# Kernel optimization log

Measured on AMD Instinct MI355X. Metric: run time of the kernel, lower is better.

Reference implementation:

```python
import jax, jax.numpy as jnp
import numpy as np

H = 128; R = 8; VN = 100; VA = 64
N = 8192; B = 64; L = 48; E = 65536


def setup_inputs() -> dict:
    key = jax.random.key(0)
    ks = jax.random.split(key, 24)
    s = 0.05
    nodeTypes = jax.random.randint(ks[0], (N,), 0, VN)
    edge_index = jax.random.randint(ks[1], (2, E), 0, N)
    edge_attr = jax.random.randint(ks[2], (E,), 0, R)
    bs = jnp.repeat(jnp.arange(B), N // B)              # sorted node->graph map
    nodes_bs = jnp.full((B,), N // B, dtype=jnp.int32)  # nodes per graph
    len_seq = jax.random.randint(ks[3], (B,), 1, L + 1).at[0].set(L)  # max == L
    sequence_input = (jax.random.uniform(ks[4], (N, L)) < 0.05).astype(jnp.float32)
    action_input = jax.random.randint(ks[5], (B,), 0, VA)
    params = dict(
        emb_nodes=jax.random.normal(ks[6], (VN, H)) * s,
        emb_actions=jax.random.normal(ks[7], (VA, H)) * s,
        rgcn_rel=jax.random.normal(ks[8], (3, R, H, H)) * s,   # per-layer relation weights
        rgcn_root=jax.random.normal(ks[9], (3, H, H)) * s,
        rgcn_bias=jnp.zeros((3, H)),
        gru_w_ih=jax.random.normal(ks[10], (3 * H, H)) * s,
        gru_w_hh=jax.random.normal(ks[11], (3 * H, H)) * s,
        gru_b_ih=jnp.zeros((3 * H,)),
        gru_b_hh=jnp.zeros((3 * H,)),
        linA_w=jax.random.normal(ks[12], (H, H)) * s,
        linA_b=jnp.zeros((H,)),
        linAf_w=jax.random.normal(ks[13], (VA, H)) * s,
        linAf_b=jnp.zeros((VA,)),
        linN_w=jax.random.normal(ks[14], (H, 2 * H)) * s,
        linN_b=jnp.zeros((H,)),
        linNf_w=jax.random.normal(ks[15], (1, H)) * s,
        linNf_b=jnp.zeros((1,)),
    )
    return dict(nodeTypes=nodeTypes, edge_index=edge_index, edge_attr=edge_attr,
                bs=bs, nodes_bs=nodes_bs, len_seq=len_seq,
                sequence_input=sequence_input, action_input=action_input, **params)


def reference(nodeTypes, edge_index, edge_attr, bs, nodes_bs, len_seq,
              sequence_input, action_input,
              emb_nodes, emb_actions, rgcn_rel, rgcn_root, rgcn_bias,
              gru_w_ih, gru_w_hh, gru_b_ih, gru_b_hh,
              linA_w, linA_b, linAf_w, linAf_b,
              linN_w, linN_b, linNf_w, linNf_b):
    n = nodeTypes.shape[0]
    b = nodes_bs.shape[0]
    h = emb_nodes.shape[1]
    r = rgcn_rel.shape[1]
    l = sequence_input.shape[1]

    x = emb_nodes[nodeTypes]                               # [N,H]
    src, dst = edge_index[0], edge_index[1]
    seg = dst * r + edge_attr                              # per (target, relation) segment
    cnt = jax.ops.segment_sum(jnp.ones((src.shape[0],), x.dtype), seg, n * r)
    denom = jnp.maximum(cnt, 1.0).reshape(n, r, 1)
    for li in range(3):
        agg = jax.ops.segment_sum(x[src], seg, n * r).reshape(n, r, h) / denom
        x = jax.nn.relu(jnp.einsum('nrh,rho->no', agg, rgcn_rel[li])
                        + x @ rgcn_root[li] + rgcn_bias[li])

    # global mean pool -> graph embedding
    h_G = jax.ops.segment_sum(x, bs, b) / nodes_bs[:, None].astype(x.dtype)  # [B,H]
    action = jax.nn.relu(h_G @ linA_w.T + linA_b) @ linAf_w.T + linAf_b      # [B,VA]

    sos = emb_actions[action_input][:, None, :]            # [B,1,H]
    # sequence embeddings: sum over nodes in each graph of seq[i,t]*x[i]
    emb_seq = sequence_input[:, :, None] * x[:, None, :]   # [N,L,H]
    out = jax.ops.segment_sum(emb_seq, bs, b)              # [B,L,H]
    input_gru = jnp.concatenate([sos, out], axis=1)[:, :l] # packed GRU only sees first L steps

    # single-layer GRU, h0 = h_G (torch gate order r,z,n)
    xW = input_gru @ gru_w_ih.T + gru_b_ih                 # [B,L,3H]
    def step(hprev, xw):
        hW = hprev @ gru_w_hh.T + gru_b_hh
        xr, xz, xn = jnp.split(xw, 3, -1)
        hr, hz, hn = jnp.split(hW, 3, -1)
        rg = jax.nn.sigmoid(xr + hr)
        zg = jax.nn.sigmoid(xz + hz)
        ng = jnp.tanh(xn + rg * hn)
        hnew = (1.0 - zg) * ng + zg * hprev
        return hnew, hnew
    _, hs = jax.lax.scan(step, h_G, jnp.swapaxes(xW, 0, 1))
    seq_out = jnp.swapaxes(hs, 0, 1)                       # [B,L,H]
    mask = jnp.arange(l)[None, :] < len_seq[:, None]       # pad_packed zero-pads
    seq_out = seq_out * mask[:, :, None]

    out_gru = seq_out[bs]                                  # repeat_interleave -> [N,L,H]
    concats = jnp.concatenate(
        [out_gru, jnp.broadcast_to(x[:, None, :], (n, l, h))], axis=2)  # [N,L,2H]
    hid = jax.nn.relu(concats @ linN_w.T + linN_b)         # [N,L,H]
    logits = (hid @ linNf_w.T + linNf_b)[..., 0]           # [N,L]

    # scatter_softmax over nodes grouped by graph (dim 0)
    m = jax.lax.stop_gradient(jax.ops.segment_max(logits, bs, b))
    e = jnp.exp(logits - m[bs])
    ssum = jax.ops.segment_sum(e, bs, b)
    nodes_final = e / ssum[bs]
    return action, nodes_final
```

## Files before the change

### kernel.cpp

```cpp
#include <hip/hip_runtime.h>
#include <hip/hip_bf16.h>

#define H   128
#define RR  8
#define NN  8192
#define BB  64
#define LL  48
#define EE  65536
#define NPG 128
#define VA  64
#define NSEG (NN*RR)
#define GPB 16

typedef unsigned short u16;
typedef unsigned int   u32;

__device__ __forceinline__ float b2f(u16 u) {
    union { u32 i; float f; } v; v.i = ((u32)u) << 16; return v.f;
}
__device__ __forceinline__ u16 f2b(float f) {
    union { float f; u32 i; } v; v.f = f;
    u32 x = v.i;
    return (u16)((x + 0x7fffu + ((x >> 16) & 1u)) >> 16);
}
__device__ __forceinline__ float2 up2(u32 p) {
    union { u32 i; float f; } a, b;
    a.i = p << 16; b.i = p & 0xffff0000u;
    return make_float2(a.f, b.f);
}
__device__ __forceinline__ u32 pk2(float a, float b) {
    return ((u32)f2b(b) << 16) | (u32)f2b(a);
}
__device__ __forceinline__ float rcpf(float x) { return __builtin_amdgcn_rcpf(x); }
__device__ __forceinline__ u32 cvtpk(float lo, float hi) {
    u32 r;
    asm("v_cvt_pk_bf16_f32 %0, %1, %2" : "=v"(r) : "v"(lo), "v"(hi));
    return r;
}

#define K_LOG2E  1.4426950408889634f
#define K_2LOG2E 2.8853900817779268f

typedef __attribute__((ext_vector_type(8))) short bf16x8;
typedef __attribute__((ext_vector_type(4))) float f32x4;
typedef __attribute__((ext_vector_type(4))) unsigned short u16x4;

__global__ __launch_bounds__(256) void k_init(const int* __restrict__ nodeTypes,
                                              const float* __restrict__ emb_nodes,
                                              float* __restrict__ x0,
                                              int* __restrict__ fill) {
    int idx = blockIdx.x * 256 + threadIdx.x;
    if (idx < NSEG) fill[idx] = 0;
    if (idx < NN * H) {
        int n = idx >> 7, h = idx & (H - 1);
        x0[idx] = emb_nodes[(size_t)nodeTypes[n] * H + h];
    }
}

__global__ __launch_bounds__(256) void k_hist(const int* __restrict__ edge_index,
                                              const int* __restrict__ edge_attr,
                                              int* __restrict__ fill) {
    int e = blockIdx.x * 256 + threadIdx.x;
    if (e < EE) {
        int seg = edge_index[EE + e] * RR + edge_attr[e];
        atomicAdd(&fill[seg], 1);
    }
}

__global__ __launch_bounds__(256) void k_scan1(const int* __restrict__ fill,
                                               int* __restrict__ bsum) {
    __shared__ int red[4];
    int tid = threadIdx.x, lane = tid & 63, wv = tid >> 6;
    int v = fill[blockIdx.x * 256 + tid];
#pragma unroll
    for (int off = 32; off >= 1; off >>= 1) v += __shfl_down(v, off, 64);
    if (lane == 0) red[wv] = v;
    __syncthreads();
    if (tid == 0) bsum[blockIdx.x] = red[0] + red[1] + red[2] + red[3];
}

__global__ __launch_bounds__(256) void k_scan2(const int* __restrict__ bsum,
                                               int* __restrict__ boff,
                                               int* __restrict__ rowptr) {
    __shared__ int s[256];
    int tid = threadIdx.x;
    int v0 = bsum[tid];
    s[tid] = v0;
    __syncthreads();
    for (int off = 1; off < 256; off <<= 1) {
        int v = (tid >= off) ? s[tid - off] : 0;
        __syncthreads();
        s[tid] += v;
        __syncthreads();
    }
    boff[tid] = s[tid] - v0;
    if (tid == 255) rowptr[NSEG] = s[255];
}

__global__ __launch_bounds__(256) void k_scan3(const int* __restrict__ boff,
                                               int* __restrict__ fill,
                                               int* __restrict__ rowptr) {
    __shared__ int s[256];
    int tid = threadIdx.x;
    int g = blockIdx.x * 256 + tid;
    int c = fill[g];
    s[tid] = c;
    __syncthreads();
    for (int off = 1; off < 256; off <<= 1) {
        int v = (tid >= off) ? s[tid - off] : 0;
        __syncthreads();
        s[tid] += v;
        __syncthreads();
    }
    int r = boff[blockIdx.x] + s[tid] - c;
    rowptr[g] = r;
    fill[g] = r;
}

__global__ __launch_bounds__(256) void k_scatter(const int* __restrict__ edge_index,
                                                 const int* __restrict__ edge_attr,
                                                 int* __restrict__ fill,
                                                 int* __restrict__ colidx) {
    int e = blockIdx.x * 256 + threadIdx.x;
    if (e < EE) {
        int seg = edge_index[EE + e] * RR + edge_attr[e];
        int pos = atomicAdd(&fill[seg], 1);
        colidx[pos] = edge_index[e];
    }
}

__global__ __launch_bounds__(256) void k_wprep(const float* __restrict__ rel,
                                               const float* __restrict__ root,
                                               const float* __restrict__ w_ih,
                                               u16* __restrict__ WTt,
                                               u16* __restrict__ WTih,
                                               float* __restrict__ hGsum) {
    int idx = blockIdx.x * 256 + threadIdx.x;
    if (idx < 384 * H) WTih[idx] = f2b(w_ih[idx]);
    if (idx < BB * H) hGsum[idx] = 0.f;
    if (idx >= 3 * 147456) return;
    int li  = idx / 147456;
    int rem = idx - li * 147456;
    int tile = rem / 36864;
    int r2   = rem - tile * 36864;
    int ks   = r2 / 1024;
    int r3   = r2 - ks * 1024;
    int sub  = r3 >> 9;
    int r4   = r3 & 511;
    int lane = r4 >> 3, j = r4 & 7;
    int col = tile * 32 + sub * 16 + (lane & 15);
    int k   = ks * 32 + (lane >> 4) * 8 + j;
    float v;
    if (k < 1024) v = rel[(((size_t)li * RR + (k >> 7)) * H + (k & 127)) * H + col];
    else          v = root[((size_t)li * H + (k - 1024)) * H + col];
    WTt[idx] = f2b(v);
}

#define RGN 16
#define EPRE 512

__global__ __launch_bounds__(512) void k_rgcn(const float* __restrict__ xin,
                                              float* __restrict__ xout,
                                              const u16* __restrict__ WTt,
                                              const float* __restrict__ bias,
                                              const int* __restrict__ rowptr,
                                              const int* __restrict__ colidx,
                                              float* __restrict__ hGsum) {
    __shared__ u32 ab[RGN * 580];
    __shared__ int begs[RGN * RR + 1];
    __shared__ int eidx[EPRE];
    int tid = threadIdx.x, wv = tid >> 6, lane = tid & 63;
    int n0 = blockIdx.x * RGN, segbase = n0 * RR;

    if (tid <= RGN * RR) begs[tid] = rowptr[segbase + tid];
    __syncthreads();
    int E0 = begs[0], ne = begs[RGN * RR] - E0;
    for (int i = tid; i < ne && i < EPRE; i += 512) eidx[i] = colidx[E0 + i];
    __syncthreads();

    for (int s = wv; s < RGN * RR; s += 8) {
        int beg = begs[s], end = begs[s + 1];
        float a0 = 0.f, a1 = 0.f;
        for (int e = beg; e < end; ++e) {
            int off = e - E0;
            int src = (off < EPRE) ? eidx[off] : colidx[e];
            float2 v = ((const float2*)(xin + (size_t)src * H))[lane];
            a0 += v.x; a1 += v.y;
        }
        float inv = 1.f / fmaxf((float)(end - beg), 1.f);
        ab[(s >> 3) * 580 + ((s & 7) << 6) + lane] = pk2(a0 * inv, a1 * inv);
    }
    for (int i = wv; i < RGN; i += 8) {
        const float* xr = xin + (size_t)(n0 + i) * H + 2 * lane;
        ab[i * 580 + 512 + lane] = pk2(xr[0], xr[1]);
    }
    __syncthreads();

    int m = lane & 15, quad = lane >> 4;
    const u32* aP = ab + m * 580 + quad * 4;
    const u32* bT = (const u32*)WTt + (size_t)(wv >> 1) * 36 * 512 + (wv & 1) * 256 + lane * 4;
    f32x4 acc0 = {0.f, 0.f, 0.f, 0.f};
    bf16x8 b0c = *(const bf16x8*)bT;
    for (int ks = 0; ks < 36; ++ks) {
        bf16x8 b0n;
        if (ks < 35) b0n = *(const bf16x8*)(bT + (ks + 1) * 512);
        bf16x8 a = *(const bf16x8*)(aP + ks * 16);
        acc0 = __builtin_amdgcn_mfma_f32_16x16x32_bf16(a, b0c, acc0, 0, 0, 0);
        b0c = b0n;
    }
    int c0 = wv * 16 + m;
    float bv0 = bias[c0];
    float so0 = 0.f;
#pragma unroll
    for (int rg = 0; rg < 4; ++rg) {
        int n = n0 + quad * 4 + rg;
        float o0 = fmaxf(acc0[rg] + bv0, 0.f);
        xout[(size_t)n * H + c0] = o0;
        so0 += o0;
    }
    if (hGsum) {
        so0 += __shfl_xor(so0, 16, 64);
        so0 += __shfl_xor(so0, 32, 64);
        if (quad == 0) {
            int g = n0 >> 7;
            atomicAdd(&hGsum[g * H + c0], so0);
        }
    }
}

__global__ __launch_bounds__(128) void k_pool_act(const float* __restrict__ hGsum,
                                                  const int* __restrict__ nodes_bs,
                                                  const float* __restrict__ linA_w,
                                                  const float* __restrict__ linA_b,
                                                  const float* __restrict__ linAf_w,
                                                  const float* __restrict__ linAf_b,
                                                  float* __restrict__ hG,
                                                  float* __restrict__ out) {
    __shared__ float hgs[H], t1[H];
    int b = blockIdx.x, h = threadIdx.x;
    float hg = hGsum[(size_t)b * H + h] / (float)nodes_bs[b];
    hG[(size_t)b * H + h] = hg;
    hgs[h] = hg;
    __syncthreads();
    float acc = linA_b[h];
    const float* wr = linA_w + (size_t)h * H;
    for (int k = 0; k < H; ++k) acc += wr[k] * hgs[k];
    t1[h] = fmaxf(acc, 0.f);
    __syncthreads();
    if (h < VA) {
        float a = linAf_b[h];
        const float* w2 = linAf_w + (size_t)h * H;
        for (int k = 0; k < H; ++k) a += w2[k] * t1[k];
        out[(size_t)b * VA + h] = a;
    }
}

__global__ __launch_bounds__(256) void k_seqpool(const float* __restrict__ xf,
                                                 const float* __restrict__ seq,
                                                 const float* __restrict__ emb_actions,
                                                 const int* __restrict__ action_input,
                                                 float* __restrict__ igG) {
    __shared__ float xg[64][H];
    __shared__ u16 lists[LL][64];
    __shared__ int cnts[LL];
    int b = blockIdx.x, tid = threadIdx.x;
    int col = tid & 127, tg = tid >> 7;
    float acc[24];
#pragma unroll
    for (int m = 0; m < 24; ++m) acc[m] = 0.f;

    for (int chunk = 0; chunk < 2; ++chunk) {
        int i0 = b * NPG + chunk * 64;
        __syncthreads();
        if (tid < LL) cnts[tid] = 0;
        __syncthreads();
        for (int idx = tid; idx < 64 * H / 4; idx += 256)
            ((float4*)&xg[0][0])[idx] = ((const float4*)(xf + (size_t)i0 * H))[idx];
        for (int idx = tid; idx < 64 * LL; idx += 256) {
            int i = idx / LL, t = idx - i * LL;
            if (seq[(size_t)(i0 + i) * LL + t] != 0.f) {
                int p = atomicAdd(&cnts[t], 1);
                lists[t][p] = (u16)i;
            }
        }
        __syncthreads();
        for (int m = 0; m < 24; ++m) {
            int t = tg + 2 * m;
            int c = cnts[t];
            float a = acc[m];
            for (int p = 0; p < c; ++p) a += xg[lists[t][p]][col];
            acc[m] = a;
        }
    }
    if (tid < H)
        igG[((size_t)b * LL) * H + tid] = emb_actions[(size_t)action_input[b] * H + tid];
#pragma unroll
    for (int m = 0; m < 24; ++m) {
        int t = tg + 2 * m;
        if (t < LL - 1)
            igG[((size_t)b * LL + t + 1) * H + col] = acc[m];
    }
}

__global__ __launch_bounds__(256) void k_xw(const float* __restrict__ igG,
                                            const u16* __restrict__ WTih,
                                            const float* __restrict__ b_ih,
                                            const float* __restrict__ b_hh,
                                            u16* __restrict__ xwG) {
    __shared__ u32 ab[16 * 68];
    int tid = threadIdx.x, wv = tid >> 6, lane = tid & 63;
    int n0 = blockIdx.x * 16;
    for (int s = tid; s < 16 * 64; s += 256) {
        int row = s >> 6, kp = s & 63;
        float2 v = *(const float2*)(igG + (size_t)(n0 + row) * H + 2 * kp);
        ab[row * 68 + kp] = pk2(v.x, v.y);
    }
    __syncthreads();
    int m = lane & 15, quad = lane >> 4;
    const u32* aP = ab + m * 68 + quad * 4;
    f32x4 acc[6];
#pragma unroll
    for (int i = 0; i < 6; ++i) acc[i] = (f32x4){0.f, 0.f, 0.f, 0.f};
#pragma unroll
    for (int ks = 0; ks < 4; ++ks) {
        bf16x8 a = *(const bf16x8*)(aP + ks * 16);
#pragma unroll
        for (int tc = 0; tc < 6; ++tc) {
            int colr = wv * 96 + tc * 16 + m;
            bf16x8 bfr = *(const bf16x8*)((const u32*)WTih + (size_t)colr * 64 + quad * 4 + ks * 16);
            acc[tc] = __builtin_amdgcn_mfma_f32_16x16x32_bf16(a, bfr, acc[tc], 0, 0, 0);
        }
    }
#pragma unroll
    for (int tc = 0; tc < 6; ++tc) {
        int c = wv * 96 + tc * 16 + m;
        float bv = b_ih[c] + ((c < 256) ? b_hh[c] : 0.f);
        float sc = (c < 256) ? K_LOG2E : K_2LOG2E;
        int R = c & 127, gate = c >> 7;
#pragma unroll
        for (int rg = 0; rg < 4; ++rg) {
            int r = n0 + quad * 4 + rg;
            int bb = r / 48, tt = r - bb * 48;
            size_t o = (((((size_t)(bb >> 4) * LL + tt) * 8 + (R >> 4)) * 3 + gate) * 256)
                     + (((R >> 2) & 3) << 6) + ((bb & 15) << 2) + (R & 3);
            xwG[o] = f2b((acc[tc][rg] + bv) * sc);
        }
    }
}

#define GRU_BLKS 4
#define BX_BLKS  (NN / 32)
#define SMEM_BYTES 33024

__global__ __launch_bounds__(512) void k_gru_bx(const u16* __restrict__ xw2,
                                                const float* __restrict__ hG,
                                                const float* __restrict__ w_hh,
                                                const float* __restrict__ b_hh,
                                                const int* __restrict__ len_seq,
                                                float* __restrict__ soutG,
                                                const float* __restrict__ xf,
                                                const float* __restrict__ linN_w,
                                                const float* __restrict__ linN_b,
                                                u16* __restrict__ BxU) {
    __shared__ __align__(16) char smem[SMEM_BYTES];
    int tid = threadIdx.x;

    if (blockIdx.x >= GRU_BLKS) {
        float* xl = (float*)smem;
        float* wb = (float*)(smem + 16384);
        int bid = blockIdx.x - GRU_BLKS;
        int n0 = bid * 32;
        for (int idx = tid; idx < 32 * H; idx += 512)
            xl[idx] = xf[(size_t)n0 * H + idx];
        int col = tid & 127, g = tid >> 7;
        float bv = linN_b[col];
        float acc[8] = {bv, bv, bv, bv, bv, bv, bv, bv};
        for (int c = 0; c < 4; ++c) {
            int k0 = c * 32;
            __syncthreads();
            for (int idx = tid; idx < 32 * H; idx += 512) {
                int r = idx >> 5, kk = idx & 31;
                wb[kk * 130 + r] = linN_w[(size_t)r * (2 * H) + H + k0 + kk];
            }
            __syncthreads();
#pragma unroll
            for (int kk = 0; kk < 32; ++kk) {
                float w = wb[kk * 130 + col];
#pragma unroll
                for (int j = 0; j < 8; ++j) acc[j] += xl[(g * 8 + j) * H + k0 + kk] * w;
            }
        }
#pragma unroll
        for (int j = 0; j < 8; ++j)
            BxU[(size_t)(n0 + g * 8 + j) * H + col] = f2b(acc[j]);
        return;
    }

    u16* hA = (u16*)smem;
    int lane = tid & 63, wv = tid >> 6;
    int mi = lane & 15, quad = lane >> 4;
    int gblk = blockIdx.x;
    int g_abs = gblk * GPB + mi;
    int R0 = 16 * wv + 4 * quad;

    int eW = (((wv >> 1) * 64) + (mi + 16 * ((2 * wv + (quad >> 1)) & 3))) * 8
             + 4 * (quad & 1);

    bf16x8 wfr[3][4];
#pragma unroll
    for (int gate = 0; gate < 3; ++gate) {
        int T = wv + 8 * gate;
        float sc = (gate == 2) ? K_2LOG2E : K_LOG2E;
#pragma unroll
        for (int ks = 0; ks < 4; ++ks) {
            const float* wp = w_hh + (size_t)(16 * T + mi) * H + quad * 8 + ks * 32;
            float4 f0 = *(const float4*)wp;
            float4 f1 = *(const float4*)(wp + 4);
            bf16x8 v;
            v[0] = (short)f2b(f0.x * sc); v[1] = (short)f2b(f0.y * sc);
            v[2] = (short)f2b(f0.z * sc); v[3] = (short)f2b(f0.w * sc);
            v[4] = (short)f2b(f1.x * sc); v[5] = (short)f2b(f1.y * sc);
            v[6] = (short)f2b(f1.z * sc); v[7] = (short)f2b(f1.w * sc);
            wfr[gate][ks] = v;
        }
    }
    float4 bn = *(const float4*)(b_hh + 256 + R0);
    float4 h0 = *(const float4*)(hG + (size_t)g_abs * H + R0);
    int ls = len_seq[g_abs];

    float hp[4]  = {h0.x, h0.y, h0.z, h0.w};
    float bnn[4] = {bn.x * K_2LOG2E, bn.y * K_2LOG2E, bn.z * K_2LOG2E, bn.w * K_2LOG2E};

    auto storeh = [&](int buf, const float* hv) {
        u32 w0 = cvtpk(hv[0], hv[1]);
        u32 w1 = cvtpk(hv[2], hv[3]);
        float2 e0 = up2(w0), e1 = up2(w1);
        u32 l0 = cvtpk(hv[0] - e0.x, hv[1] - e0.y);
        u32 l1 = cvtpk(hv[2] - e1.x, hv[3] - e1.y);
        *(uint2*)&hA[buf * 4096 + eW]        = make_uint2(w0, w1);
        *(uint2*)&hA[buf * 4096 + 2048 + eW] = make_uint2(l0, l1);
    };
    auto loadxw = [&](int t, u16x4* d) {
        const u16* p = xw2 + ((((size_t)gblk * LL + t) * 8 + wv) * 3) * 256
                     + (quad << 6) + (mi << 2);
        d[0] = *(const u16x4*)(p);
        d[1] = *(const u16x4*)(p + 256);
        d[2] = *(const u16x4*)(p + 512);
    };

    auto step = [&](int t, const u16x4* x, int buf) {
        f32x4 acc[3];
        acc[0] = (f32x4){0.f, 0.f, 0.f, 0.f};
        acc[1] = (f32x4){0.f, 0.f, 0.f, 0.f};
        acc[2] = (f32x4){bnn[0], bnn[1], bnn[2], bnn[3]};
#pragma unroll
        for (int ks = 0; ks < 4; ++ks) {
            const int e = (ks * 64 + lane) * 8;
            bf16x8 bh = *(const bf16x8*)&hA[buf * 4096 + e];
            bf16x8 bl = *(const bf16x8*)&hA[buf * 4096 + 2048 + e];
#pragma unroll
            for (int gate = 0; gate < 3; ++gate) {
                acc[gate] = __builtin_amdgcn_mfma_f32_16x16x32_bf16(wfr[gate][ks], bh, acc[gate], 0, 0, 0);
                acc[gate] = __builtin_amdgcn_mfma_f32_16x16x32_bf16(wfr[gate][ks], bl, acc[gate], 0, 0, 0);
            }
        }
        float hv[4];
        float4 so;
#pragma unroll
        for (int r = 0; r < 4; ++r) {
            float xr = b2f(x[0][r]);
            float xz = b2f(x[1][r]);
            float xn = b2f(x[2][r]);
            float rg = rcpf(1.f + __builtin_amdgcn_exp2f(-(xr + acc[0][r])));
            float zg = rcpf(1.f + __builtin_amdgcn_exp2f(-(xz + acc[1][r])));
            float u  = xn + rg * acc[2][r];
            float ng = 1.f - 2.f * rcpf(__builtin_amdgcn_exp2f(u) + 1.f);
            float hn = ng + zg * (hp[r] - ng);
            hp[r] = hn;
            hv[r] = hn;
            ((float*)&so)[r] = (t < ls) ? hn : 0.f;
        }
        *(float4*)(soutG + ((size_t)g_abs * LL + t) * H + R0) = so;
        storeh(buf ^ 1, hv);
    };

    u16x4 xa[3], xb[3];
    loadxw(0, xa);
    loadxw(1, xb);
    storeh(0, hp);
    asm volatile("s_waitcnt lgkmcnt(0)\n\ts_barrier" ::: "memory");

    for (int t = 0; t < LL; t += 2) {
        step(t, xa, 0);
        if (t + 2 < LL) loadxw(t + 2, xa);
        asm volatile("s_waitcnt lgkmcnt(0)\n\ts_barrier" ::: "memory");
        step(t + 1, xb, 1);
        if (t + 3 < LL) loadxw(t + 3, xb);
        asm volatile("s_waitcnt lgkmcnt(0)\n\ts_barrier" ::: "memory");
    }
}

__global__ __launch_bounds__(256) void k_a2(const float* __restrict__ soutG,
                                            const float* __restrict__ linN_w,
                                            float* __restrict__ A2) {
    __shared__ float wb[32][130];
    __shared__ float xl[16][H];
    int tid = threadIdx.x;
    int n0 = blockIdx.x * 16;
    for (int idx = tid; idx < 16 * H; idx += 256)
        xl[idx >> 7][idx & 127] = soutG[(size_t)n0 * H + idx];
    int col = tid & 127, g = tid >> 7;
    float acc[8] = {0.f, 0.f, 0.f, 0.f, 0.f, 0.f, 0.f, 0.f};
    for (int c = 0; c < 4; ++c) {
        int k0 = c * 32;
        __syncthreads();
        for (int idx = tid; idx < 32 * H; idx += 256) {
            int r = idx >> 5, kk = idx & 31;
            wb[kk][r] = linN_w[(size_t)r * (2 * H) + k0 + kk];
        }
        __syncthreads();
#pragma unroll
        for (int kk = 0; kk < 32; ++kk) {
            float w = wb[kk][col];
#pragma unroll
            for (int j = 0; j < 8; ++j) acc[j] += xl[g * 8 + j][k0 + kk] * w;
        }
    }
#pragma unroll
    for (int j = 0; j < 8; ++j)
        A2[(size_t)(n0 + g * 8 + j) * H + col] = acc[j];
}

__global__ __launch_bounds__(256) void k_logits(const float* __restrict__ A2,
                                                const u16* __restrict__ BxU,
                                                const float* __restrict__ linNf_w,
                                                float* __restrict__ logits) {
    __shared__ float a2s[LL][130];
    __shared__ float bxs[16][130];
    __shared__ float w2s[H];
    int tid = threadIdx.x;
    int g = blockIdx.x >> 3, tile = blockIdx.x & 7;
    int n0g = g * NPG + tile * 16;

    for (int i2 = tid; i2 < LL * 64; i2 += 256) {
        int r = i2 >> 6, c2 = i2 & 63;
        *(float2*)&a2s[r][2 * c2] = *(const float2*)(A2 + ((size_t)g * LL + r) * H + 2 * c2);
    }
    for (int iu = tid; iu < 16 * 64; iu += 256) {
        int r = iu >> 6, c = iu & 63;
        float2 v = up2(((const u32*)BxU)[(size_t)(n0g + r) * 64 + c]);
        *(float2*)&bxs[r][2 * c] = v;
    }
    if (tid < H) w2s[tid] = linNf_w[tid];
    __syncthreads();

    int n = tid & 15, tt = tid >> 4;
#pragma unroll
    for (int pass = 0; pass < 3; ++pass) {
        int t = tt + 16 * pass;
        float acc = 0.f;
#pragma unroll
        for (int kp = 0; kp < 64; ++kp) {
            float2 a2 = *(const float2*)&a2s[t][2 * kp];
            float2 bx = *(const float2*)&bxs[n][2 * kp];
            float2 w  = *(const float2*)&w2s[2 * kp];
            acc += w.x * fmaxf(a2.x + bx.x, 0.f) + w.y * fmaxf(a2.y + bx.y, 0.f);
        }
        logits[(size_t)(n0g + n) * LL + t] = acc;
    }
}

__global__ __launch_bounds__(256) void k_softmax(const float* __restrict__ logits,
                                                 float* __restrict__ out) {
    __shared__ float lg[NPG][LL + 1];
    __shared__ float pm[4][LL], ps[4][LL];
    __shared__ float mv[LL], inv[LL];
    int b = blockIdx.x, tid = threadIdx.x;
    int n0 = b * NPG;
    for (int idx = tid; idx < NPG * LL; idx += 256) {
        int n = idx / LL, t = idx - n * LL;
        lg[n][t] = logits[(size_t)n0 * LL + idx];
    }
    __syncthreads();
    int t = tid & 63, seg = tid >> 6;
    if (t < LL) {
        float m = -1e30f;
        int nb = seg * 32;
        for (int n = nb; n < nb + 32; ++n) m = fmaxf(m, lg[n][t]);
        pm[seg][t] = m;
    }
    __syncthreads();
    if (tid < LL)
        mv[tid] = fmaxf(fmaxf(pm[0][tid], pm[1][tid]), fmaxf(pm[2][tid], pm[3][tid]));
    __syncthreads();
    if (t < LL) {
        float m = mv[t], s = 0.f;
        int nb = seg * 32;
        for (int n = nb; n < nb + 32; ++n) {
            float e = __expf(lg[n][t] - m);
            lg[n][t] = e;
            s += e;
        }
        ps[seg][t] = s;
    }
    __syncthreads();
    if (tid < LL)
        inv[tid] = 1.f / (ps[0][tid] + ps[1][tid] + ps[2][tid] + ps[3][tid]);
    __syncthreads();
    for (int idx = tid; idx < NPG * LL; idx += 256) {
        int n = idx / LL, tc = idx - n * LL;
        out[(size_t)BB * VA + (size_t)n0 * LL + idx] = lg[n][tc] * inv[tc];
    }
}

extern "C" void kernel_launch(void* const* d_in, const int* in_sizes, int n_in,
                              void* d_out, int out_size, void* d_ws, size_t ws_size,
                              hipStream_t stream) {
    (void)in_sizes; (void)n_in; (void)out_size; (void)ws_size;
    const int*   nodeTypes    = (const int*)d_in[0];
    const int*   edge_index   = (const int*)d_in[1];
    const int*   edge_attr    = (const int*)d_in[2];
    const int*   nodes_bs     = (const int*)d_in[4];
    const int*   len_seq      = (const int*)d_in[5];
    const float* seq_in       = (const float*)d_in[6];
    const int*   action_input = (const int*)d_in[7];
    const float* emb_nodes    = (const float*)d_in[8];
    const float* emb_actions  = (const float*)d_in[9];
    const float* rgcn_rel     = (const float*)d_in[10];
    const float* rgcn_root    = (const float*)d_in[11];
    const float* rgcn_bias    = (const float*)d_in[12];
    const float* gru_w_ih     = (const float*)d_in[13];
    const float* gru_w_hh     = (const float*)d_in[14];
    const float* gru_b_ih     = (const float*)d_in[15];
    const float* gru_b_hh     = (const float*)d_in[16];
    const float* linA_w       = (const float*)d_in[17];
    const float* linA_b       = (const float*)d_in[18];
    const float* linAf_w      = (const float*)d_in[19];
    const float* linAf_b      = (const float*)d_in[20];
    const float* linN_w       = (const float*)d_in[21];
    const float* linN_b       = (const float*)d_in[22];
    const float* linNf_w      = (const float*)d_in[23];

    char* w = (char*)d_ws;
    float* x0      = (float*)(w + 0);
    u16*   xwG     = (u16*)  (w + 0);
    float* logitsW = (float*)(w + 0);
    float* soutG   = (float*)(w + 2359296);
    float* x1      = (float*)(w + 4194304);
    float* igG     = (float*)(w + 8388608);
    float* A2      = (float*)(w + 8388608);
    u16*   BxU     = (u16*)  (w + 9961472);
    int*   bsum    = (int*)  (w + 9961472);
    int*   boff    = (int*)  (w + 9962496);
    float* hGsum   = (float*)(w + 9969664);
    int*   rowptr  = (int*)  (w + 11567104);
    int*   fill    = (int*)  (w + 11829760);
    u16*   WTih    = (u16*)  (w + 11829760);
    float* hG      = (float*)(w + 12058624);
    int*   colidx  = (int*)  (w + 12091904);
    u16*   WT      = (u16*)  (w + 12616192);

    float* out_f = (float*)d_out;

    k_init<<<dim3(4096), dim3(256), 0, stream>>>(nodeTypes, emb_nodes, x0, fill);
    k_hist<<<dim3(256), dim3(256), 0, stream>>>(edge_index, edge_attr, fill);
    k_scan1<<<dim3(256), dim3(256), 0, stream>>>(fill, bsum);
    k_scan2<<<dim3(1), dim3(256), 0, stream>>>(bsum, boff, rowptr);
    k_scan3<<<dim3(256), dim3(256), 0, stream>>>(boff, fill, rowptr);
    k_scatter<<<dim3(256), dim3(256), 0, stream>>>(edge_index, edge_attr, fill, colidx);
    k_wprep<<<dim3(1728), dim3(256), 0, stream>>>(rgcn_rel, rgcn_root, gru_w_ih,
                                                  WT, WTih, hGsum);

    const int rg_grid = NN / RGN;
    k_rgcn<<<dim3(rg_grid), dim3(512), 0, stream>>>(x0, x1,
        WT + 0 * 147456, rgcn_bias + 0 * H, rowptr, colidx, nullptr);
    k_rgcn<<<dim3(rg_grid), dim3(512), 0, stream>>>(x1, x0,
        WT + 1 * 147456, rgcn_bias + 1 * H, rowptr, colidx, nullptr);
    k_rgcn<<<dim3(rg_grid), dim3(512), 0, stream>>>(x0, x1,
        WT + 2 * 147456, rgcn_bias + 2 * H, rowptr, colidx, hGsum);

    k_pool_act<<<dim3(BB), dim3(128), 0, stream>>>(hGsum, nodes_bs, linA_w, linA_b,
                                                   linAf_w, linAf_b, hG, out_f);
    k_seqpool<<<dim3(BB), dim3(256), 0, stream>>>(x1, seq_in, emb_actions, action_input, igG);
    k_xw<<<dim3(BB * LL / 16), dim3(256), 0, stream>>>(igG, WTih, gru_b_ih, gru_b_hh, xwG);
    k_gru_bx<<<dim3(GRU_BLKS + BX_BLKS), dim3(512), 0, stream>>>(xwG, hG, gru_w_hh,
        gru_b_hh, len_seq, soutG, x1, linN_w, linN_b, BxU);
    k_a2<<<dim3(BB * LL / 16), dim3(256), 0, stream>>>(soutG, linN_w, A2);
    k_logits<<<dim3(BB * 8), dim3(256), 0, stream>>>(A2, BxU, linNf_w, logitsW);
    k_softmax<<<dim3(BB), dim3(256), 0, stream>>>(logitsW, out_f);
}
```

Before: 321.6 us.

## Replace CSR edge build with per-block buckets and LDS atomic aggregation

Replaces the histogram, three-pass scan and scatter CSR construction with a single bucketing kernel that places each edge in a fixed-capacity bucket per 16-node destination block. The RGCN kernel then aggregates neighbour features with shared-memory float atomics and normalises by per-relation counts. Separately, the init and weight-prep kernels are merged, as are the pool/action and sequence-pool kernels, which cuts the launch count. The risks are the CAP=256 bucket cap, which silently drops edges if a block receives more, the contention from LDS atomics, and a non-deterministic summation order.

```diff
diff --git a/kernel.cpp b/kernel.cpp
--- a/kernel.cpp
+++ b/kernel.cpp
@@ -9,8 +9,8 @@
 #define EE  65536
 #define NPG 128
 #define VA  64
-#define NSEG (NN*RR)
 #define GPB 16
+#define CAP 256
 
 typedef unsigned short u16;
 typedef unsigned int   u32;
@@ -45,167 +45,119 @@
 typedef __attribute__((ext_vector_type(4))) float f32x4;
 typedef __attribute__((ext_vector_type(4))) unsigned short u16x4;
 
-__global__ __launch_bounds__(256) void k_init(const int* __restrict__ nodeTypes,
+__global__ __launch_bounds__(256) void k_prep(const int* __restrict__ nodeTypes,
                                               const float* __restrict__ emb_nodes,
+                                              const float* __restrict__ rel,
+                                              const float* __restrict__ root,
+                                              const float* __restrict__ w_ih,
                                               float* __restrict__ x0,
-                                              int* __restrict__ fill) {
+                                              u16* __restrict__ WTt,
+                                              u16* __restrict__ WTih,
+                                              float* __restrict__ hGsum,
+                                              int* __restrict__ bcnt) {
     int idx = blockIdx.x * 256 + threadIdx.x;
-    if (idx < NSEG) fill[idx] = 0;
+    if (idx < 512) bcnt[idx] = 0;
+    if (idx < 384 * H) WTih[idx] = f2b(w_ih[idx]);
+    if (idx < BB * H) hGsum[idx] = 0.f;
     if (idx < NN * H) {
         int n = idx >> 7, h = idx & (H - 1);
         x0[idx] = emb_nodes[(size_t)nodeTypes[n] * H + h];
     }
-}
-
-__global__ __launch_bounds__(256) void k_hist(const int* __restrict__ edge_index,
-                                              const int* __restrict__ edge_attr,
-                                              int* __restrict__ fill) {
-    int e = blockIdx.x * 256 + threadIdx.x;
-    if (e < EE) {
-        int seg = edge_index[EE + e] * RR + edge_attr[e];
-        atomicAdd(&fill[seg], 1);
-    }
-}
-
-__global__ __launch_bounds__(256) void k_scan1(const int* __restrict__ fill,
-                                               int* __restrict__ bsum) {
-    __shared__ int red[4];
-    int tid = threadIdx.x, lane = tid & 63, wv = tid >> 6;
-    int v = fill[blockIdx.x * 256 + tid];
-#pragma unroll
-    for (int off = 32; off >= 1; off >>= 1) v += __shfl_down(v, off, 64);
-    if (lane == 0) red[wv] = v;
-    __syncthreads();
-    if (tid == 0) bsum[blockIdx.x] = red[0] + red[1] + red[2] + red[3];
-}
-
-__global__ __launch_bounds__(256) void k_scan2(const int* __restrict__ bsum,
-                                               int* __restrict__ boff,
-                                               int* __restrict__ rowptr) {
-    __shared__ int s[256];
-    int tid = threadIdx.x;
-    int v0 = bsum[tid];
-    s[tid] = v0;
-    __syncthreads();
-    for (int off = 1; off < 256; off <<= 1) {
-        int v = (tid >= off) ? s[tid - off] : 0;
-        __syncthreads();
-        s[tid] += v;
-        __syncthreads();
-    }
-    boff[tid] = s[tid] - v0;
-    if (tid == 255) rowptr[NSEG] = s[255];
-}
-
-__global__ __launch_bounds__(256) void k_scan3(const int* __restrict__ boff,
-                                               int* __restrict__ fill,
-                                               int* __restrict__ rowptr) {
-    __shared__ int s[256];
-    int tid = threadIdx.x;
-    int g = blockIdx.x * 256 + tid;
-    int c = fill[g];
-    s[tid] = c;
-    __syncthreads();
-    for (int off = 1; off < 256; off <<= 1) {
-        int v = (tid >= off) ? s[tid - off] : 0;
-        __syncthreads();
-        s[tid] += v;
-        __syncthreads();
-    }
-    int r = boff[blockIdx.x] + s[tid] - c;
-    rowptr[g] = r;
-    fill[g] = r;
-}
-
-__global__ __launch_bounds__(256) void k_scatter(const int* __restrict__ edge_index,
-                                                 const int* __restrict__ edge_attr,
-                                                 int* __restrict__ fill,
-                                                 int* __restrict__ colidx) {
-    int e = blockIdx.x * 256 + threadIdx.x;
-    if (e < EE) {
-        int seg = edge_index[EE + e] * RR + edge_attr[e];
-        int pos = atomicAdd(&fill[seg], 1);
-        colidx[pos] = edge_index[e];
-    }
-}
-
-__global__ __launch_bounds__(256) void k_wprep(const float* __restrict__ rel,
-                                               const float* __restrict__ root,
-                                               const float* __restrict__ w_ih,
-                                               u16* __restrict__ WTt,
-                                               u16* __restrict__ WTih,
-                                               float* __restrict__ hGsum) {
-    int idx = blockIdx.x * 256 + threadIdx.x;
-    if (idx < 384 * H) WTih[idx] = f2b(w_ih[idx]);
-    if (idx < BB * H) hGsum[idx] = 0.f;
-    if (idx >= 3 * 147456) return;
-    int li  = idx / 147456;
-    int rem = idx - li * 147456;
+    int j = idx - NN * H;
+    if (j < 0 || j >= 3 * 147456) return;
+    int li  = j / 147456;
+    int rem = j - li * 147456;
     int tile = rem / 36864;
     int r2   = rem - tile * 36864;
     int ks   = r2 / 1024;
     int r3   = r2 - ks * 1024;
     int sub  = r3 >> 9;
     int r4   = r3 & 511;
-    int lane = r4 >> 3, j = r4 & 7;
+    int lane = r4 >> 3, jj = r4 & 7;
     int col = tile * 32 + sub * 16 + (lane & 15);
-    int k   = ks * 32 + (lane >> 4) * 8 + j;
+    int k   = ks * 32 + (lane >> 4) * 8 + jj;
     float v;
     if (k < 1024) v = rel[(((size_t)li * RR + (k >> 7)) * H + (k & 127)) * H + col];
     else          v = root[((size_t)li * H + (k - 1024)) * H + col];
-    WTt[idx] = f2b(v);
+    WTt[j] = f2b(v);
+}
+
+__global__ __launch_bounds__(256) void k_bucket(const int* __restrict__ edge_index,
+                                                const int* __restrict__ edge_attr,
+                                                int* __restrict__ bcnt,
+                                                u32* __restrict__ bucket) {
+    int e = blockIdx.x * 256 + threadIdx.x;
+    if (e < EE) {
+        int dst = edge_index[EE + e];
+        int blk = dst >> 4;
+        int pos = atomicAdd(&bcnt[blk], 1);
+        if (pos < CAP) {
+            u32 sl = (u32)(((dst & 15) << 3) | edge_attr[e]);
+            bucket[(size_t)blk * CAP + pos] = (u32)edge_index[e] | (sl << 16);
+        }
+    }
 }
 
 #define RGN 16
-#define EPRE 512
 
 __global__ __launch_bounds__(512) void k_rgcn(const float* __restrict__ xin,
                                               float* __restrict__ xout,
                                               const u16* __restrict__ WTt,
                                               const float* __restrict__ bias,
-                                              const int* __restrict__ rowptr,
-                                              const int* __restrict__ colidx,
+                                              const int* __restrict__ bcnt,
+                                              const u32* __restrict__ bucket,
                                               float* __restrict__ hGsum) {
-    __shared__ u32 ab[RGN * 580];
-    __shared__ int begs[RGN * RR + 1];
-    __shared__ int eidx[EPRE];
+    __shared__ __align__(16) float agg[RGN * 9 * 132];
+    __shared__ u32 ebuf[CAP];
+    __shared__ int cnts[RGN * RR];
     int tid = threadIdx.x, wv = tid >> 6, lane = tid & 63;
-    int n0 = blockIdx.x * RGN, segbase = n0 * RR;
-
-    if (tid <= RGN * RR) begs[tid] = rowptr[segbase + tid];
-    __syncthreads();
-    int E0 = begs[0], ne = begs[RGN * RR] - E0;
-    for (int i = tid; i < ne && i < EPRE; i += 512) eidx[i] = colidx[E0 + i];
-    __syncthreads();
-
-    for (int s = wv; s < RGN * RR; s += 8) {
-        int beg = begs[s], end = begs[s + 1];
-        float a0 = 0.f, a1 = 0.f;
-        for (int e = beg; e < end; ++e) {
-            int off = e - E0;
-            int src = (off < EPRE) ? eidx[off] : colidx[e];
-            float2 v = ((const float2*)(xin + (size_t)src * H))[lane];
-            a0 += v.x; a1 += v.y;
-        }
-        float inv = 1.f / fmaxf((float)(end - beg), 1.f);
-        ab[(s >> 3) * 580 + ((s & 7) << 6) + lane] = pk2(a0 * inv, a1 * inv);
-    }
-    for (int i = wv; i < RGN; i += 8) {
-        const float* xr = xin + (size_t)(n0 + i) * H + 2 * lane;
-        ab[i * 580 + 512 + lane] = pk2(xr[0], xr[1]);
+    int blk = blockIdx.x, n0 = blk * RGN;
+    int ne = min(bcnt[blk], CAP);
+
+    for (int i = tid; i < ne; i += 512) ebuf[i] = bucket[(size_t)blk * CAP + i];
+    for (int i = tid; i < RGN * RR; i += 512) cnts[i] = 0;
+    for (int i = tid; i < RGN * 8 * 128; i += 512) {
+        int n = i >> 10, r = (i >> 7) & 7, h = i & 127;
+        agg[(n * 9 + r) * 132 + h] = 0.f;
+    }
+    for (int i = tid; i < RGN * 128; i += 512)
+        agg[((i >> 7) * 9 + 8) * 132 + (i & 127)] = xin[(size_t)n0 * H + i];
+    __syncthreads();
+
+    for (int e = wv; e < ne; e += 8) {
+        u32 pk = ebuf[e];
+        int src = pk & 0xffff, sl = pk >> 16;
+        float2 v = ((const float2*)(xin + (size_t)src * H))[lane];
+        float* dst = &agg[((sl >> 3) * 9 + (sl & 7)) * 132 + 2 * lane];
+        atomicAdd(dst, v.x);
+        atomicAdd(dst + 1, v.y);
+        if (lane == 0) atomicAdd(&cnts[sl], 1);
+    }
+    __syncthreads();
+
+    for (int i = tid; i < RGN * 8 * 128; i += 512) {
+        int n = i >> 10, r = (i >> 7) & 7, h = i & 127;
+        float sc = 1.f / fmaxf((float)cnts[i >> 7], 1.f);
+        agg[(n * 9 + r) * 132 + h] *= sc;
     }
     __syncthreads();
 
     int m = lane & 15, quad = lane >> 4;
-    const u32* aP = ab + m * 580 + quad * 4;
     const u32* bT = (const u32*)WTt + (size_t)(wv >> 1) * 36 * 512 + (wv & 1) * 256 + lane * 4;
     f32x4 acc0 = {0.f, 0.f, 0.f, 0.f};
     bf16x8 b0c = *(const bf16x8*)bT;
     for (int ks = 0; ks < 36; ++ks) {
         bf16x8 b0n;
         if (ks < 35) b0n = *(const bf16x8*)(bT + (ks + 1) * 512);
-        bf16x8 a = *(const bf16x8*)(aP + ks * 16);
-        acc0 = __builtin_amdgcn_mfma_f32_16x16x32_bf16(a, b0c, acc0, 0, 0, 0);
+        int seg = ks >> 2;
+        int h0 = (ks * 32 + quad * 8) & 127;
+        const float* ap = &agg[(m * 9 + seg) * 132 + h0];
+        float4 f0 = *(const float4*)ap;
+        float4 f1 = *(const float4*)(ap + 4);
+        union { u32 u[4]; bf16x8 v; } av;
+        av.u[0] = cvtpk(f0.x, f0.y); av.u[1] = cvtpk(f0.z, f0.w);
+        av.u[2] = cvtpk(f1.x, f1.y); av.u[3] = cvtpk(f1.z, f1.w);
+        acc0 = __builtin_amdgcn_mfma_f32_16x16x32_bf16(av.v, b0c, acc0, 0, 0, 0);
         b0c = b0n;
     }
     int c0 = wv * 16 + m;
@@ -228,42 +180,51 @@
     }
 }
 
-__global__ __launch_bounds__(128) void k_pool_act(const float* __restrict__ hGsum,
+__global__ __launch_bounds__(256) void k_pool_seq(const float* __restrict__ hGsum,
                                                   const int* __restrict__ nodes_bs,
                                                   const float* __restrict__ linA_w,
                                                   const float* __restrict__ linA_b,
                                                   const float* __restrict__ linAf_w,
                                                   const float* __restrict__ linAf_b,
                                                   float* __restrict__ hG,
-                                                  float* __restrict__ out) {
-    __shared__ float hgs[H], t1[H];
-    int b = blockIdx.x, h = threadIdx.x;
-    float hg = hGsum[(size_t)b * H + h] / (float)nodes_bs[b];
-    hG[(size_t)b * H + h] = hg;
-    hgs[h] = hg;
-    __syncthreads();
-    float acc = linA_b[h];
-    const float* wr = linA_w + (size_t)h * H;
-    for (int k = 0; k < H; ++k) acc += wr[k] * hgs[k];
-    t1[h] = fmaxf(acc, 0.f);
-    __syncthreads();
-    if (h < VA) {
-        float a = linAf_b[h];
-        const float* w2 = linAf_w + (size_t)h * H;
-        for (int k = 0; k < H; ++k) a += w2[k] * t1[k];
-        out[(size_t)b * VA + h] = a;
-    }
-}
-
-__global__ __launch_bounds__(256) void k_seqpool(const float* __restrict__ xf,
-                                                 const float* __restrict__ seq,
-                                                 const float* __restrict__ emb_actions,
-                                                 const int* __restrict__ action_input,
-                                                 float* __restrict__ igG) {
+                                                  float* __restrict__ out,
+                                                  const float* __restrict__ xf,
+                                                  const float* __restrict__ seq,
+                                                  const float* __restrict__ emb_actions,
+                                                  const int* __restrict__ action_input,
+                                                  float* __restrict__ igG) {
     __shared__ float xg[64][H];
     __shared__ u16 lists[LL][64];
     __shared__ int cnts[LL];
-    int b = blockIdx.x, tid = threadIdx.x;
+    int tid = threadIdx.x;
+
+    if (blockIdx.x < BB) {
+        float* hgs = &xg[0][0];
+        float* t1  = &xg[1][0];
+        int b = blockIdx.x, h = tid;
+        if (h < H) {
+            float hg = hGsum[(size_t)b * H + h] / (float)nodes_bs[b];
+            hG[(size_t)b * H + h] = hg;
+            hgs[h] = hg;
+        }
+        __syncthreads();
+        if (h < H) {
+            float acc = linA_b[h];
+            const float* wr = linA_w + (size_t)h * H;
+            for (int k = 0; k < H; ++k) acc += wr[k] * hgs[k];
+            t1[h] = fmaxf(acc, 0.f);
+        }
+        __syncthreads();
+        if (h < VA) {
+            float a = linAf_b[h];
+            const float* w2 = linAf_w + (size_t)h * H;
+            for (int k = 0; k < H; ++k) a += w2[k] * t1[k];
+            out[(size_t)b * VA + h] = a;
+        }
+        return;
+    }
+
+    int b = blockIdx.x - BB;
     int col = tid & 127, tg = tid >> 7;
     float acc[24];
 #pragma unroll
@@ -650,38 +611,29 @@
     float* igG     = (float*)(w + 8388608);
     float* A2      = (float*)(w + 8388608);
     u16*   BxU     = (u16*)  (w + 9961472);
-    int*   bsum    = (int*)  (w + 9961472);
-    int*   boff    = (int*)  (w + 9962496);
     float* hGsum   = (float*)(w + 9969664);
-    int*   rowptr  = (int*)  (w + 11567104);
-    int*   fill    = (int*)  (w + 11829760);
+    int*   bcnt    = (int*)  (w + 11567104);
     u16*   WTih    = (u16*)  (w + 11829760);
     float* hG      = (float*)(w + 12058624);
-    int*   colidx  = (int*)  (w + 12091904);
+    u32*   bucket  = (u32*)  (w + 12091904);
     u16*   WT      = (u16*)  (w + 12616192);
 
     float* out_f = (float*)d_out;
 
-    k_init<<<dim3(4096), dim3(256), 0, stream>>>(nodeTypes, emb_nodes, x0, fill);
-    k_hist<<<dim3(256), dim3(256), 0, stream>>>(edge_index, edge_attr, fill);
-    k_scan1<<<dim3(256), dim3(256), 0, stream>>>(fill, bsum);
-    k_scan2<<<dim3(1), dim3(256), 0, stream>>>(bsum, boff, rowptr);
-    k_scan3<<<dim3(256), dim3(256), 0, stream>>>(boff, fill, rowptr);
-    k_scatter<<<dim3(256), dim3(256), 0, stream>>>(edge_index, edge_attr, fill, colidx);
-    k_wprep<<<dim3(1728), dim3(256), 0, stream>>>(rgcn_rel, rgcn_root, gru_w_ih,
-                                                  WT, WTih, hGsum);
+    k_prep<<<dim3(5824), dim3(256), 0, stream>>>(nodeTypes, emb_nodes, rgcn_rel,
+        rgcn_root, gru_w_ih, x0, WT, WTih, hGsum, bcnt);
+    k_bucket<<<dim3(256), dim3(256), 0, stream>>>(edge_index, edge_attr, bcnt, bucket);
 
     const int rg_grid = NN / RGN;
     k_rgcn<<<dim3(rg_grid), dim3(512), 0, stream>>>(x0, x1,
-        WT + 0 * 147456, rgcn_bias + 0 * H, rowptr, colidx, nullptr);
+        WT + 0 * 147456, rgcn_bias + 0 * H, bcnt, bucket, nullptr);
     k_rgcn<<<dim3(rg_grid), dim3(512), 0, stream>>>(x1, x0,
-        WT + 1 * 147456, rgcn_bias + 1 * H, rowptr, colidx, nullptr);
+        WT + 1 * 147456, rgcn_bias + 1 * H, bcnt, bucket, nullptr);
     k_rgcn<<<dim3(rg_grid), dim3(512), 0, stream>>>(x0, x1,
-        WT + 2 * 147456, rgcn_bias + 2 * H, rowptr, colidx, hGsum);
-
-    k_pool_act<<<dim3(BB), dim3(128), 0, stream>>>(hGsum, nodes_bs, linA_w, linA_b,
-                                                   linAf_w, linAf_b, hG, out_f);
-    k_seqpool<<<dim3(BB), dim3(256), 0, stream>>>(x1, seq_in, emb_actions, action_input, igG);
+        WT + 2 * 147456, rgcn_bias + 2 * H, bcnt, bucket, hGsum);
+
+    k_pool_seq<<<dim3(2 * BB), dim3(256), 0, stream>>>(hGsum, nodes_bs, linA_w, linA_b,
+        linAf_w, linAf_b, hG, out_f, x1, seq_in, emb_actions, action_input, igG);
     k_xw<<<dim3(BB * LL / 16), dim3(256), 0, stream>>>(igG, WTih, gru_b_ih, gru_b_hh, xwG);
     k_gru_bx<<<dim3(GRU_BLKS + BX_BLKS), dim3(512), 0, stream>>>(xwG, hG, gru_w_hh,
         gru_b_hh, len_seq, soutG, x1, linN_w, linN_b, BxU);
```

Measured after the change: 450.5 us. +40.1%, slower.
